# Performance work log

Hardware: AMD Instinct MI355X
Metric: run time of the kernel (lower is better)

Reference implementation:

```python
import jax, jax.numpy as jnp
from jax import lax
import numpy as np


def conv2d(x, w, b=None, stride=1, pad=0, groups=1):
    out = lax.conv_general_dilated(x, w, (stride, stride), [(pad, pad), (pad, pad)],
                                   dimension_numbers=('NCHW', 'OIHW', 'NCHW'),
                                   feature_group_count=groups)
    if b is not None:
        out = out + b[None, :, None, None]
    return out


def ln(x, g, b, eps=1e-5):
    m = x.mean(-1, keepdims=True)
    v = ((x - m) ** 2).mean(-1, keepdims=True)
    return (x - m) * lax.rsqrt(v + eps) * g + b


def grid_sample_bilinear(img, grid):
    # img [N,C,H,W]; grid [N,Hg,Wg,2] with (x,y) in [-1,1]; align_corners=True, zeros padding
    N, C, H, W = img.shape
    x = (grid[..., 0] + 1.0) * 0.5 * (W - 1)
    y = (grid[..., 1] + 1.0) * 0.5 * (H - 1)
    x0 = jnp.floor(x); y0 = jnp.floor(y)
    x1 = x0 + 1.0; y1 = y0 + 1.0
    wx1 = x - x0; wx0 = 1.0 - wx1
    wy1 = y - y0; wy0 = 1.0 - wy1
    imgh = img.transpose(0, 2, 3, 1)  # [N,H,W,C]
    bidx = jnp.arange(N)[:, None, None]
    def g(ix, iy):
        valid = (ix >= 0) & (ix <= W - 1) & (iy >= 0) & (iy <= H - 1)
        ixc = jnp.clip(ix, 0, W - 1).astype(jnp.int32)
        iyc = jnp.clip(iy, 0, H - 1).astype(jnp.int32)
        return imgh[bidx, iyc, ixc] * valid[..., None].astype(img.dtype)
    out = (g(x0, y0) * (wx0 * wy0)[..., None] + g(x1, y0) * (wx1 * wy0)[..., None]
           + g(x0, y1) * (wx0 * wy1)[..., None] + g(x1, y1) * (wx1 * wy1)[..., None])
    return out.transpose(0, 3, 1, 2)  # [N,C,Hg,Wg]


def setup_inputs() -> dict:
    key = jax.random.key(0)
    ks = iter(jax.random.split(key, 64))
    def rn(shape, s=0.02):
        return jax.random.normal(next(ks), shape, jnp.float32) * s
    B, C, H, W = 4, 512, 32, 32
    gc, hid = 256, 1024
    d = {}
    d['feat_tgt'] = jax.random.normal(next(ks), (B, C, H, W), jnp.float32)
    d['feat_ref'] = jax.random.normal(next(ks), (B, C, H, W), jnp.float32)
    d['emb_w'] = rn((C, 2 * C, 3, 3)); d['emb_b'] = jnp.zeros((C,), jnp.float32)
    d['q_w'] = rn((C, C)); d['q_b'] = jnp.zeros((C,), jnp.float32)
    d['k_w'] = rn((C, C)); d['k_b'] = jnp.zeros((C,), jnp.float32)
    d['v_w'] = rn((C, C)); d['v_b'] = jnp.zeros((C,), jnp.float32)
    d['out_w'] = rn((C, C)); d['out_b'] = jnp.zeros((C,), jnp.float32)
    d['ln1_w'] = jnp.ones((gc,), jnp.float32); d['ln1_b'] = jnp.zeros((gc,), jnp.float32)
    d['mb_n1_w'] = jnp.ones((gc,), jnp.float32); d['mb_n1_b'] = jnp.zeros((gc,), jnp.float32)
    d['mb_q_w'] = rn((gc, gc)); d['mb_q_b'] = jnp.zeros((gc,), jnp.float32)
    d['mb_kv_w'] = rn((2 * gc, gc)); d['mb_kv_b'] = jnp.zeros((2 * gc,), jnp.float32)
    d['mb_proj_w'] = rn((gc, gc)); d['mb_proj_b'] = jnp.zeros((gc,), jnp.float32)
    d['mb_n2_w'] = jnp.ones((gc,), jnp.float32); d['mb_n2_b'] = jnp.zeros((gc,), jnp.float32)
    d['mb_fc1_w'] = rn((hid, gc)); d['mb_fc1_b'] = jnp.zeros((hid,), jnp.float32)
    d['mb_dw_w'] = rn((hid, 1, 3, 3)); d['mb_dw_b'] = jnp.zeros((hid,), jnp.float32)
    d['mb_fc2_w'] = rn((gc, hid)); d['mb_fc2_b'] = jnp.zeros((gc,), jnp.float32)
    d['co_dw_w'] = rn((gc, 1, 9, 9)); d['co_dw_b'] = jnp.zeros((gc,), jnp.float32)
    d['co_ln_w'] = jnp.ones((gc,), jnp.float32); d['co_ln_b'] = jnp.zeros((gc,), jnp.float32)
    d['co_out_w'] = rn((2, gc))
    return d


def reference(feat_tgt, feat_ref, emb_w, emb_b, q_w, q_b, k_w, k_b, v_w, v_b, out_w, out_b,
              ln1_w, ln1_b, mb_n1_w, mb_n1_b, mb_q_w, mb_q_b, mb_kv_w, mb_kv_b,
              mb_proj_w, mb_proj_b, mb_n2_w, mb_n2_b, mb_fc1_w, mb_fc1_b, mb_dw_w, mb_dw_b,
              mb_fc2_w, mb_fc2_b, co_dw_w, co_dw_b, co_ln_w, co_ln_b, co_out_w):
    B, C, H, W = feat_tgt.shape
    G = 2                      # n_groups
    gc = C // G                # n_group_channels
    heads, hc = 8, C // 8      # n_heads, n_head_channels
    # embedding conv over concat(target, reference)
    feat = conv2d(jnp.concatenate([feat_tgt, feat_ref], 1), emb_w, emb_b, pad=1)
    q = jnp.einsum('bchw,oc->bohw', feat_tgt, q_w) + q_b[None, :, None, None]
    # group tokens + LN
    fg = feat.reshape(B * G, gc, H * W).transpose(0, 2, 1)  # [BG, N, gc]
    x = ln(fg, ln1_w, ln1_b)
    # ---- MitBlock offset generator ----
    BG, N, D = x.shape
    mh = 8; mhd = D // mh
    h = ln(x, mb_n1_w, mb_n1_b, 1e-6)
    qq = (h @ mb_q_w.T + mb_q_b).reshape(BG, N, mh, mhd).transpose(0, 2, 1, 3)
    kv = (h @ mb_kv_w.T + mb_kv_b).reshape(BG, N, 2, mh, mhd).transpose(2, 0, 3, 1, 4)
    kk, vv = kv[0], kv[1]
    a = jax.nn.softmax(jnp.einsum('bhnd,bhmd->bhnm', qq, kk) * (mhd ** -0.5), axis=-1)
    o = jnp.einsum('bhnm,bhmd->bhnd', a, vv).transpose(0, 2, 1, 3).reshape(BG, N, D)
    x = x + (o @ mb_proj_w.T + mb_proj_b)
    h2 = ln(x, mb_n2_w, mb_n2_b, 1e-6)
    m = h2 @ mb_fc1_w.T + mb_fc1_b                         # [BG, N, hid]
    hid = m.shape[-1]
    mi = m.transpose(0, 2, 1).reshape(BG, hid, H, W)
    mi = conv2d(mi, mb_dw_w, mb_dw_b, pad=1, groups=hid)
    m = jax.nn.gelu(mi.reshape(BG, hid, N).transpose(0, 2, 1), approximate=False)
    x = x + (m @ mb_fc2_w.T + mb_fc2_b)
    # ---- conv_offset stack ----
    off = x.reshape(BG, H, W, gc).transpose(0, 3, 1, 2)
    off = conv2d(off, co_dw_w, co_dw_b, pad=4, groups=gc)
    off = ln(off.transpose(0, 2, 3, 1), co_ln_w, co_ln_b).transpose(0, 3, 1, 2)
    off = jax.nn.gelu(off, approximate=False)
    off = jnp.einsum('bchw,oc->bohw', off, co_out_w)       # [BG, 2, Hk, Wk]
    Hk, Wk = off.shape[2], off.shape[3]
    ns = Hk * Wk
    rng = jnp.array([1.0 / Hk, 1.0 / Wk], feat.dtype).reshape(1, 2, 1, 1)
    off = jnp.tanh(off) * rng * 2.0                        # offset_range_factor = 2
    off = off.transpose(0, 2, 3, 1)                        # [BG, Hk, Wk, 2] (y,x)
    ry = (jnp.linspace(0.5, Hk - 0.5, Hk, dtype=feat.dtype) / Hk) * 2 - 1
    rx = (jnp.linspace(0.5, Wk - 0.5, Wk, dtype=feat.dtype) / Wk) * 2 - 1
    ref = jnp.stack(jnp.meshgrid(ry, rx, indexing='ij'), -1)  # [Hk, Wk, 2] (y,x)
    pos = off + ref[None]
    sampled = grid_sample_bilinear(feat.reshape(BG, gc, H, W), pos[..., ::-1])
    sampled = sampled.reshape(B, C, ns)
    k = jnp.einsum('bcn,oc->bon', sampled, k_w) + k_b[None, :, None]
    v = jnp.einsum('bcn,oc->bon', sampled, v_w) + v_b[None, :, None]
    qh = q.reshape(B * heads, hc, H * W)
    kh = k.reshape(B * heads, hc, ns)
    vh = v.reshape(B * heads, hc, ns)
    attn = jax.nn.softmax(jnp.einsum('bcm,bcn->bmn', qh, kh) * (hc ** -0.5), axis=-1)
    out = jnp.einsum('bmn,bcn->bcm', attn, vh).reshape(B, C, H, W)
    y = jnp.einsum('bchw,oc->bohw', out, out_w) + out_b[None, :, None, None]
    return y
```

## Files before the change

### kernel.cpp

```cpp
#include <hip/hip_runtime.h>
#include <math.h>


static constexpr int HW = 1024;

typedef __attribute__((ext_vector_type(8))) short bf16x8;
typedef __attribute__((ext_vector_type(4))) float f32x4;

union V16u { int4 i4; ushort u[8]; };

__device__ __forceinline__ float gelu_exact(float v) {
  return 0.5f * v * (1.0f + erff(v * 0.7071067811865475f));
}

__device__ __forceinline__ ushort bf16_rne(float v) {
  unsigned int b = __float_as_uint(v);
  return (ushort)((b + 0x7fffu + ((b >> 16) & 1u)) >> 16);
}

__device__ __forceinline__ void split2(float v, ushort& h, ushort& l) {
  h = bf16_rne(v);
  l = bf16_rne(v - __uint_as_float(((unsigned int)h) << 16));
}

__device__ __forceinline__ void wfrag_body(const float* __restrict__ W, int K, int KC,
                                           ushort* __restrict__ dh, ushort* __restrict__ dl,
                                           int gtid, float scale) {
  int l = gtid & 63; int fr = gtid >> 6;
  int kc = fr % KC; int ot = fr / KC;
  int lr = l & 15, lu = l >> 4;
  const float* sp = W + (size_t)(ot * 16 + lr) * K + kc * 32 + lu * 8;
  V16u hi, lo;
#pragma unroll
  for (int j = 0; j < 8; ++j) split2(sp[j] * scale, hi.u[j], lo.u[j]);
  *(int4*)(dh + (size_t)gtid * 8) = hi.i4;
  *(int4*)(dl + (size_t)gtid * 8) = lo.i4;
}

__global__ void k_prep_all(
    const float* __restrict__ emb_w, const float* __restrict__ tgt,
    const float* __restrict__ refp,
    const float* q_w, const float* k_w, const float* v_w, const float* o_w,
    const float* mq_w, const float* mkv_w, const float* mp_w,
    const float* f1_w, const float* f2_w, const float* dw9_w,
    const float* q_b, const float* mq_b, const float* mkv_b,
    const float* k_b, const float* v_b,
    ushort* __restrict__ WtEH, ushort* __restrict__ WtEL,
    ushort* __restrict__ XtH, ushort* __restrict__ XtL,
    ushort* qh, ushort* ql, ushort* kvh, ushort* kvl,
    ushort* oh, ushort* ol, ushort* mqkvh, ushort* mqkvl,
    ushort* mph, ushort* mpl, ushort* f1h, ushort* f1l, ushort* f2h, ushort* f2l,
    float* wt9, float* biasmb, float* biaskv, float* biasq,
    ushort* tgtfh, ushort* tgtfl) {
  int bid = blockIdx.x, tid = threadIdx.x;
  if (bid < 2048) {
    int idx = bid * 256 + tid;
    int o = idx >> 10, ci = idx & 1023;
    const float* src = emb_w + (size_t)idx * 9;
#pragma unroll
    for (int t = 0; t < 9; ++t) {
      ushort h, l; split2(src[t], h, l);
      size_t oo = ((size_t)(t * 512 + o)) * 1024 + ci;
      WtEH[oo] = h; WtEL[oo] = l;
    }
  } else if (bid < 4360) {
    int idx = (bid - 2048) * 256 + tid;
    int xp = idx % 34; int r = idx / 34;
    int g8 = r & 127; r >>= 7;
    int yp = r % 34; int b = r / 34;
    int y = yp - 1, x = xp - 1;
    bool valid = (unsigned)y < 32u && (unsigned)x < 32u;
    V16u hi, lo;
    const float* in = (g8 < 64) ? (tgt + ((size_t)(b * 512 + g8 * 8)) * HW)
                                : (refp + ((size_t)(b * 512 + (g8 - 64) * 8)) * HW);
#pragma unroll
    for (int j = 0; j < 8; ++j) {
      float v = valid ? in[(size_t)j * HW + y * 32 + x] : 0.f;
      split2(v, hi.u[j], lo.u[j]);
    }
    size_t oo = (((size_t)(b * 34 + yp)) * 34 + xp) * 1024 + g8 * 8;
    *(int4*)(XtH + oo) = hi.i4;
    *(int4*)(XtL + oo) = lo.i4;
  }
  else if (bid < 4488) wfrag_body(q_w, 512, 16, qh, ql, (bid - 4360) * 256 + tid, 0.125f);
  else if (bid < 4616) wfrag_body(k_w, 512, 16, kvh, kvl, (bid - 4488) * 256 + tid, 1.f);
  else if (bid < 4744) wfrag_body(v_w, 512, 16, kvh + 262144, kvl + 262144,
                                  (bid - 4616) * 256 + tid, 1.f);
  else if (bid < 4872) wfrag_body(o_w, 512, 16, oh, ol, (bid - 4744) * 256 + tid, 1.f);
  else if (bid < 4904) wfrag_body(mq_w, 256, 8, mqkvh, mqkvl, (bid - 4872) * 256 + tid,
                                  0.17677669529663689f);
  else if (bid < 4968) wfrag_body(mkv_w, 256, 8, mqkvh + 65536, mqkvl + 65536,
                                  (bid - 4904) * 256 + tid, 1.f);
  else if (bid < 5000) wfrag_body(mp_w, 256, 8, mph, mpl, (bid - 4968) * 256 + tid, 1.f);
  else if (bid < 5128) wfrag_body(f1_w, 256, 8, f1h, f1l, (bid - 5000) * 256 + tid, 1.f);
  else if (bid < 5256) wfrag_body(f2_w, 1024, 32, f2h, f2l, (bid - 5128) * 256 + tid, 1.f);
  else if (bid < 5337) {
    int idx = (bid - 5256) * 256 + tid;
    int t = idx >> 8, c = idx & 255;
    wt9[idx] = dw9_w[c * 81 + t];
  } else if (bid < 5346) {
    int idx = (bid - 5337) * 256 + tid;
    if (idx < 768)
      biasmb[idx] = idx < 256 ? mq_b[idx] * 0.17677669529663689f : mkv_b[idx - 256];
    else if (idx < 1792) {
      int j = idx - 768;
      biaskv[j] = j < 512 ? k_b[j] : v_b[j - 512];
    } else if (idx < 2304) {
      biasq[idx - 1792] = q_b[idx - 1792] * 0.125f;
    }
  } else {
    int gtid = (bid - 5346) * 256 + tid;
    int l = gtid & 63; int fr = gtid >> 6;
    int kc = fr % 16; int r2 = fr / 16; int nt = r2 & 63; int b = r2 >> 6;
    int lr = l & 15, lu = l >> 4;
    const float* sp = tgt + ((size_t)(b * 512) + kc * 32 + lu * 8) * 1024 + nt * 16 + lr;
    V16u hi, lo;
#pragma unroll
    for (int j = 0; j < 8; ++j) split2(sp[(size_t)j * 1024], hi.u[j], lo.u[j]);
    *(int4*)(tgtfh + (size_t)gtid * 8) = hi.i4;
    *(int4*)(tgtfl + (size_t)gtid * 8) = lo.i4;
  }
}

__global__ __launch_bounds__(256, 2)
void k_emb_mfma(const ushort* __restrict__ Xt_hi, const ushort* __restrict__ Xt_lo,
                const ushort* __restrict__ Wt_hi, const ushort* __restrict__ Wt_lo,
                float* __restrict__ part) {
  int wgid = (blockIdx.x & 7) * 64 + (blockIdx.x >> 3);
  int yt = wgid & 7;  wgid >>= 3;
  int b  = wgid & 3;  wgid >>= 2;
  int mt = wgid & 3;  wgid >>= 2;
  int ks = wgid;
  int tid = threadIdx.x;
  int w = tid >> 6, l = tid & 63;
  int lr = l & 15, lu = l >> 4;
  int y0 = yt * 4;
  int obase = mt * 128 + w * 32;

  __shared__ int4 LsH[2][816];
  __shared__ int4 LsL[2][816];

  int4 gh[4], gl[4];
  int kc0 = ks * 8;

  auto loadstage = [&](int kcg) {
#pragma unroll
    for (int i = 0; i < 4; ++i) {
      int s = tid + 256 * i;
      if (s < 816) {
        int px = s >> 2;
        int u = (s & 3) ^ ((px >> 1) & 3);
        size_t off = ((size_t)(b * 34 + y0) * 34 + px) * 1024 + kcg * 32 + u * 8;
        gh[i] = *(const int4*)(Xt_hi + off);
        gl[i] = *(const int4*)(Xt_lo + off);
      }
    }
  };
  auto writestage = [&](int buf) {
#pragma unroll
    for (int i = 0; i < 4; ++i) {
      int s = tid + 256 * i;
      if (s < 816) { LsH[buf][s] = gh[i]; LsL[buf][s] = gl[i]; }
    }
  };

  f32x4 zero = {0.f, 0.f, 0.f, 0.f};
  f32x4 acc[2][8];
#pragma unroll
  for (int a = 0; a < 2; ++a)
#pragma unroll
    for (int n = 0; n < 8; ++n) acc[a][n] = zero;

  loadstage(kc0);
  writestage(0);

  for (int kc = 0; kc < 8; ++kc) {
    int buf = kc & 1;
    __syncthreads();
    if (kc < 7) loadstage(kc0 + kc + 1);
    int kcg = kc0 + kc;
    const bf16x8* BH = (const bf16x8*)&LsH[buf][0];
    const bf16x8* BL = (const bf16x8*)&LsL[buf][0];
#pragma unroll
    for (int kx = 0; kx < 3; ++kx) {
      bf16x8 bh[12], bl[12];
#pragma unroll
      for (int f = 0; f < 12; ++f) {
        int px = (f >> 1) * 34 + (f & 1) * 16 + kx + lr;
        int idx = px * 4 + (lu ^ ((px >> 1) & 3));
        bh[f] = BH[idx]; bl[f] = BL[idx];
      }
#pragma unroll
      for (int ky = 0; ky < 3; ++ky) {
        int tap = ky * 3 + kx;
        size_t wo = (((size_t)(tap * 512 + obase + lr)) * 1024) + kcg * 32 + lu * 8;
        bf16x8 ah0 = *(const bf16x8*)(Wt_hi + wo);
        bf16x8 al0 = *(const bf16x8*)(Wt_lo + wo);
        bf16x8 ah1 = *(const bf16x8*)(Wt_hi + wo + 16 * 1024);
        bf16x8 al1 = *(const bf16x8*)(Wt_lo + wo + 16 * 1024);
#pragma unroll
        for (int yr = 0; yr < 4; ++yr)
#pragma unroll
          for (int h = 0; h < 2; ++h) {
            int f = (yr + ky) * 2 + h;
            int nf = yr * 2 + h;
            acc[0][nf] = __builtin_amdgcn_mfma_f32_16x16x32_bf16(ah0, bh[f], acc[0][nf], 0, 0, 0);
            acc[0][nf] = __builtin_amdgcn_mfma_f32_16x16x32_bf16(ah0, bl[f], acc[0][nf], 0, 0, 0);
            acc[0][nf] = __builtin_amdgcn_mfma_f32_16x16x32_bf16(al0, bh[f], acc[0][nf], 0, 0, 0);
            acc[1][nf] = __builtin_amdgcn_mfma_f32_16x16x32_bf16(ah1, bh[f], acc[1][nf], 0, 0, 0);
            acc[1][nf] = __builtin_amdgcn_mfma_f32_16x16x32_bf16(ah1, bl[f], acc[1][nf], 0, 0, 0);
            acc[1][nf] = __builtin_amdgcn_mfma_f32_16x16x32_bf16(al1, bh[f], acc[1][nf], 0, 0, 0);
          }
      }
    }
    if (kc < 7) writestage(buf ^ 1);
  }

  float* pb = part + (size_t)ks * 2097152;
#pragma unroll
  for (int a = 0; a < 2; ++a)
#pragma unroll
    for (int yr = 0; yr < 4; ++yr)
#pragma unroll
      for (int h = 0; h < 2; ++h) {
        f32x4 c = acc[a][yr * 2 + h];
        size_t base = ((size_t)(b * 512 + obase + a * 16 + lu * 4)) * 1024
                      + (y0 + yr) * 32 + h * 16 + lr;
#pragma unroll
        for (int r = 0; r < 4; ++r) pb[base + (size_t)r * 1024] = c[r];
      }
}

__global__ void k_embmerge_nc(const float* __restrict__ part, const float* __restrict__ bias,
                              float* __restrict__ featnc) {
  __shared__ float T[64][65];
  int bid = blockIdx.x;
  int n0 = (bid & 15) << 6; bid >>= 4;
  int c0 = (bid & 3) << 6; int bg = bid >> 2;
  int cl = threadIdx.x & 63, rw = threadIdx.x >> 6;
#pragma unroll
  for (int i = 0; i < 16; ++i) {
    int crow = i * 4 + rw;
    size_t idx = ((size_t)(bg * 256 + c0 + crow)) * 1024 + n0 + cl;
    float v = part[idx] + part[2097152 + idx] + part[4194304 + idx] + part[6291456 + idx];
    T[crow][cl] = v + bias[(bg & 1) * 256 + c0 + crow];
  }
  __syncthreads();
#pragma unroll
  for (int i = 0; i < 16; ++i) {
    int nrow = i * 4 + rw;
    featnc[((size_t)(bg * 1024 + n0 + nrow)) * 256 + c0 + cl] = T[cl][nrow];
  }
}

__global__ __launch_bounds__(256)
void k_gemm_mfma(const ushort* __restrict__ Ah, const ushort* __restrict__ Al,
                 const ushort* __restrict__ Bh, const ushort* __restrict__ Bl,
                 const float* __restrict__ bias, float* __restrict__ Y,
                 int KC, int MT, int Mtot) {
  int bid = blockIdx.x;
  int ntb = bid & 15; bid >>= 4;
  int mt = bid % MT; int b = bid / MT;
  int tid = threadIdx.x, w = tid >> 6, l = tid & 63, lr = l & 15, lu = l >> 4;
  int wo = w >> 1, wn = w & 1;
  int ot0 = mt * 4 + wo * 2;
  int nf0 = ntb * 4 + wn * 2;
  const bf16x8* pAh = (const bf16x8*)Ah;
  const bf16x8* pAl = (const bf16x8*)Al;
  const bf16x8* pBh = (const bf16x8*)Bh;
  const bf16x8* pBl = (const bf16x8*)Bl;
  f32x4 zero = {0.f, 0.f, 0.f, 0.f};
  f32x4 acc[2][2];
#pragma unroll
  for (int a = 0; a < 2; ++a)
#pragma unroll
    for (int n = 0; n < 2; ++n) acc[a][n] = zero;
  for (int kc = 0; kc < KC; ++kc) {
    bf16x8 a_h[2], a_l[2];
#pragma unroll
    for (int a = 0; a < 2; ++a) {
      size_t idx = ((size_t)(ot0 + a) * KC + kc) * 64 + l;
      a_h[a] = pAh[idx]; a_l[a] = pAl[idx];
    }
#pragma unroll
    for (int n = 0; n < 2; ++n) {
      size_t idx = (((size_t)(b * 64 + nf0 + n)) * KC + kc) * 64 + l;
      bf16x8 b_h = pBh[idx], b_l = pBl[idx];
#pragma unroll
      for (int a = 0; a < 2; ++a) {
        acc[a][n] = __builtin_amdgcn_mfma_f32_16x16x32_bf16(a_h[a], b_h, acc[a][n], 0, 0, 0);
        acc[a][n] = __builtin_amdgcn_mfma_f32_16x16x32_bf16(a_h[a], b_l, acc[a][n], 0, 0, 0);
        acc[a][n] = __builtin_amdgcn_mfma_f32_16x16x32_bf16(a_l[a], b_h, acc[a][n], 0, 0, 0);
      }
    }
  }
#pragma unroll
  for (int a = 0; a < 2; ++a) {
    int o = (ot0 + a) * 16 + lu * 4;
#pragma unroll
    for (int n = 0; n < 2; ++n) {
      int col = (nf0 + n) * 16 + lr;
#pragma unroll
      for (int r = 0; r < 4; ++r)
        Y[((size_t)(b * Mtot + o + r)) * 1024 + col] = acc[a][n][r] + bias[o + r];
    }
  }
}

__global__ __launch_bounds__(256)
void k_gemm_resadd(const ushort* __restrict__ Ah, const ushort* __restrict__ Al,
                   const ushort* __restrict__ Bh, const ushort* __restrict__ Bl,
                   const float* __restrict__ bias, const float* __restrict__ res,
                   float* __restrict__ dst, int KC, int MT, int addmode) {
  int bid = blockIdx.x;
  int ntb = bid & 15; bid >>= 4;
  int mt = bid % MT; int b = bid / MT;
  int tid = threadIdx.x, w = tid >> 6, l = tid & 63, lr = l & 15, lu = l >> 4;
  int wo = w >> 1, wn = w & 1;
  int ot0 = mt * 4 + wo * 2;
  int nf0 = ntb * 4 + wn * 2;
  const bf16x8* pAh = (const bf16x8*)Ah;
  const bf16x8* pAl = (const bf16x8*)Al;
  const bf16x8* pBh = (const bf16x8*)Bh;
  const bf16x8* pBl = (const bf16x8*)Bl;
  f32x4 zero = {0.f, 0.f, 0.f, 0.f};
  f32x4 acc[2][2];
#pragma unroll
  for (int a = 0; a < 2; ++a)
#pragma unroll
    for (int n = 0; n < 2; ++n) acc[a][n] = zero;
  for (int kc = 0; kc < KC; ++kc) {
    bf16x8 a_h[2], a_l[2];
#pragma unroll
    for (int a = 0; a < 2; ++a) {
      size_t idx = ((size_t)(ot0 + a) * KC + kc) * 64 + l;
      a_h[a] = pAh[idx]; a_l[a] = pAl[idx];
    }
#pragma unroll
    for (int n = 0; n < 2; ++n) {
      size_t idx = (((size_t)(b * 64 + nf0 + n)) * KC + kc) * 64 + l;
      bf16x8 b_h = pBh[idx], b_l = pBl[idx];
#pragma unroll
      for (int a = 0; a < 2; ++a) {
        acc[a][n] = __builtin_amdgcn_mfma_f32_16x16x32_bf16(a_h[a], b_h, acc[a][n], 0, 0, 0);
        acc[a][n] = __builtin_amdgcn_mfma_f32_16x16x32_bf16(a_h[a], b_l, acc[a][n], 0, 0, 0);
        acc[a][n] = __builtin_amdgcn_mfma_f32_16x16x32_bf16(a_l[a], b_h, acc[a][n], 0, 0, 0);
      }
    }
  }
#pragma unroll
  for (int a = 0; a < 2; ++a) {
    int o = (ot0 + a) * 16 + lu * 4;
#pragma unroll
    for (int n = 0; n < 2; ++n) {
      int col = (nf0 + n) * 16 + lr;
      size_t addr = ((size_t)((b << 10) + col)) * 256 + o;
      float4 v;
      v.x = acc[a][n][0] + bias[o + 0];
      v.y = acc[a][n][1] + bias[o + 1];
      v.z = acc[a][n][2] + bias[o + 2];
      v.w = acc[a][n][3] + bias[o + 3];
      float4 r4 = addmode ? *(const float4*)(dst + addr) : *(const float4*)(res + addr);
      v.x += r4.x; v.y += r4.y; v.z += r4.z; v.w += r4.w;
      *(float4*)(dst + addr) = v;
    }
  }
}

__global__ __launch_bounds__(256)
void k_gemm_frag_mb(const ushort* __restrict__ Ah, const ushort* __restrict__ Al,
                    const ushort* __restrict__ Bh, const ushort* __restrict__ Bl,
                    const float* __restrict__ bias,
                    ushort* __restrict__ mQh, ushort* __restrict__ mQl,
                    ushort* __restrict__ mKh, ushort* __restrict__ mKl,
                    ushort* __restrict__ mVh, ushort* __restrict__ mVl) {
  int bid = blockIdx.x;
  int ntb = bid & 15; bid >>= 4;
  int mt = bid % 12; int b = bid / 12;
  int tid = threadIdx.x, w = tid >> 6, l = tid & 63, lr = l & 15, lu = l >> 4;
  int wo = w >> 1, wn = w & 1;
  int ot0 = mt * 4 + wo * 2;
  int nf0 = ntb * 4 + wn * 2;
  const bf16x8* pAh = (const bf16x8*)Ah;
// ... 231 lines not shown
        den += (p0 + p1) + (p2 + p3);
        ushort h0, l0, h1, l1, h2, l2, h3, l3;
        split2(p0, h0, l0); split2(p1, h1, l1); split2(p2, h2, l2); split2(p3, h3, l3);
        uh.x = (unsigned)h0 | ((unsigned)h1 << 16); uh.y = (unsigned)h2 | ((unsigned)h3 << 16);
        ul.x = (unsigned)l0 | ((unsigned)l1 << 16); ul.y = (unsigned)l2 | ((unsigned)l3 << 16);
      }
      *(uint2*)&Ph[w][lr][kt4 * 16 + lu * 4] = uh;
      *(uint2*)&Pl[w][lr][kt4 * 16 + lu * 4] = ul;
    }
#pragma unroll
    for (int kc2 = 0; kc2 < 2; ++kc2) {
      int kc = kb * 2 + kc2;
      bf16x8 bph = *(const bf16x8*)&Ph[w][lr][kc2 * 32 + lu * 8];
      bf16x8 bpl = *(const bf16x8*)&Pl[w][lr][kc2 * 32 + lu * 8];
#pragma unroll
      for (int et = 0; et < 2; ++et) {
        bf16x8 vh = ((const bf16x8*)Vh)[(size_t)((bgh * 2 + et) * 32 + kc) * 64 + l];
        bf16x8 vl = ((const bf16x8*)Vl)[(size_t)((bgh * 2 + et) * 32 + kc) * 64 + l];
        oacc[et] = __builtin_amdgcn_mfma_f32_16x16x32_bf16(vh, bph, oacc[et], 0, 0, 0);
        oacc[et] = __builtin_amdgcn_mfma_f32_16x16x32_bf16(vh, bpl, oacc[et], 0, 0, 0);
        oacc[et] = __builtin_amdgcn_mfma_f32_16x16x32_bf16(vl, bph, oacc[et], 0, 0, 0);
      }
    }
  }
  den += __shfl_xor(den, 16);
  den += __shfl_xor(den, 32);
  float inv = 1.f / den;
  int bg = bgh >> 3, hh = bgh & 7;
#pragma unroll
  for (int et = 0; et < 2; ++et) {
    ushort4 h4, l4;
    split2(oacc[et][0] * inv, h4.x, l4.x); split2(oacc[et][1] * inv, h4.y, l4.y);
    split2(oacc[et][2] * inv, h4.z, l4.z); split2(oacc[et][3] * inv, h4.w, l4.w);
    int lu_f = et * 2 + (lu >> 1), j0 = (lu & 1) * 4;
    size_t base = ((((size_t)(bg * 64 + qt)) * 8 + hh) * 64 + lu_f * 16 + lr) * 8 + j0;
    *(ushort4*)(ofh + base) = h4;
    *(ushort4*)(ofl + base) = l4;
  }
}

__global__ __launch_bounds__(256)
void k_mainattn_mfma(const ushort* __restrict__ Qh, const ushort* __restrict__ Ql,
                     const ushort* __restrict__ Kh, const ushort* __restrict__ Kl,
                     const ushort* __restrict__ Vh, const ushort* __restrict__ Vl,
                     ushort* __restrict__ anfh, ushort* __restrict__ anfl) {
  int qb = blockIdx.x & 15, bh = blockIdx.x >> 4;
  int tid = threadIdx.x, w = tid >> 6, l = tid & 63, lr = l & 15, lu = l >> 4;
  int qt = qb * 4 + w;
  bf16x8 qh[2], ql[2];
#pragma unroll
  for (int dc = 0; dc < 2; ++dc) {
    qh[dc] = ((const bf16x8*)Qh)[(size_t)((bh * 64 + qt) * 2 + dc) * 64 + l];
    ql[dc] = ((const bf16x8*)Ql)[(size_t)((bh * 64 + qt) * 2 + dc) * 64 + l];
  }
  __shared__ ushort Ph[4][16][72];
  __shared__ ushort Pl[4][16][72];
  f32x4 zero = {0.f, 0.f, 0.f, 0.f};
  f32x4 oacc[4] = {zero, zero, zero, zero};
  float den = 0.f;
  for (int kb = 0; kb < 16; ++kb) {
#pragma unroll
    for (int kt4 = 0; kt4 < 4; ++kt4) {
      int kt = kb * 4 + kt4;
      f32x4 s = zero;
#pragma unroll
      for (int dc = 0; dc < 2; ++dc) {
        bf16x8 kh = ((const bf16x8*)Kh)[(size_t)((bh * 64 + kt) * 2 + dc) * 64 + l];
        bf16x8 kl = ((const bf16x8*)Kl)[(size_t)((bh * 64 + kt) * 2 + dc) * 64 + l];
        s = __builtin_amdgcn_mfma_f32_16x16x32_bf16(kh, qh[dc], s, 0, 0, 0);
        s = __builtin_amdgcn_mfma_f32_16x16x32_bf16(kh, ql[dc], s, 0, 0, 0);
        s = __builtin_amdgcn_mfma_f32_16x16x32_bf16(kl, qh[dc], s, 0, 0, 0);
      }
      uint2 uh, ul;
      {
        float p0 = __expf(s[0]), p1 = __expf(s[1]), p2 = __expf(s[2]), p3 = __expf(s[3]);
        den += (p0 + p1) + (p2 + p3);
        ushort h0, l0, h1, l1, h2, l2, h3, l3;
        split2(p0, h0, l0); split2(p1, h1, l1); split2(p2, h2, l2); split2(p3, h3, l3);
        uh.x = (unsigned)h0 | ((unsigned)h1 << 16); uh.y = (unsigned)h2 | ((unsigned)h3 << 16);
        ul.x = (unsigned)l0 | ((unsigned)l1 << 16); ul.y = (unsigned)l2 | ((unsigned)l3 << 16);
      }
      *(uint2*)&Ph[w][lr][kt4 * 16 + lu * 4] = uh;
      *(uint2*)&Pl[w][lr][kt4 * 16 + lu * 4] = ul;
    }
#pragma unroll
    for (int kc2 = 0; kc2 < 2; ++kc2) {
      int kc = kb * 2 + kc2;
      bf16x8 bph = *(const bf16x8*)&Ph[w][lr][kc2 * 32 + lu * 8];
      bf16x8 bpl = *(const bf16x8*)&Pl[w][lr][kc2 * 32 + lu * 8];
#pragma unroll
      for (int et = 0; et < 4; ++et) {
        bf16x8 vh = ((const bf16x8*)Vh)[(size_t)((bh * 4 + et) * 32 + kc) * 64 + l];
        bf16x8 vl = ((const bf16x8*)Vl)[(size_t)((bh * 4 + et) * 32 + kc) * 64 + l];
        oacc[et] = __builtin_amdgcn_mfma_f32_16x16x32_bf16(vh, bph, oacc[et], 0, 0, 0);
        oacc[et] = __builtin_amdgcn_mfma_f32_16x16x32_bf16(vh, bpl, oacc[et], 0, 0, 0);
        oacc[et] = __builtin_amdgcn_mfma_f32_16x16x32_bf16(vl, bph, oacc[et], 0, 0, 0);
      }
    }
  }
  den += __shfl_xor(den, 16);
  den += __shfl_xor(den, 32);
  float inv = 1.f / den;
  int b = bh >> 3, h = bh & 7;
#pragma unroll
  for (int et = 0; et < 4; ++et) {
    ushort4 h4, l4;
    split2(oacc[et][0] * inv, h4.x, l4.x); split2(oacc[et][1] * inv, h4.y, l4.y);
    split2(oacc[et][2] * inv, h4.z, l4.z); split2(oacc[et][3] * inv, h4.w, l4.w);
    int kc = h * 2 + (et >> 1);
    int lu_f = (et & 1) * 2 + (lu >> 1), j0 = (lu & 1) * 4;
    size_t base = ((((size_t)(b * 64 + qt)) * 16 + kc) * 64 + lu_f * 16 + lr) * 8 + j0;
    *(ushort4*)(anfh + base) = h4;
    *(ushort4*)(anfl + base) = l4;
  }
}

__global__ void k_dw3_frag(const float* __restrict__ X, const float* __restrict__ w,
                           const float* __restrict__ bias,
                           ushort* __restrict__ dh, ushort* __restrict__ dl) {
  int bid = blockIdx.x;
  int pch = bid & 3; bid >>= 2;
  int chg = bid & 127; int bg = bid >> 7;
  int tid = threadIdx.x;
  int n = pch * 256 + tid;
  int x = n & 31, y = n >> 5;
  int ch0 = chg * 8;
  V16u hi, lo;
#pragma unroll
  for (int jj = 0; jj < 8; ++jj) {
    int ch = ch0 + jj;
    const float* src = X + ((size_t)((bg << 10) + ch)) * HW;
    const float* wr = w + ch * 9;
    float acc = bias[ch];
#pragma unroll
    for (int ky = 0; ky < 3; ++ky) {
      int yy = y + ky - 1;
      if ((unsigned)yy < 32u) {
        const float* row = src + yy * 32;
#pragma unroll
        for (int kx = 0; kx < 3; ++kx) {
          int xx = x + kx - 1;
          if ((unsigned)xx < 32u) acc += row[xx] * wr[ky * 3 + kx];
        }
      }
    }
    split2(gelu_exact(acc), hi.u[jj], lo.u[jj]);
  }
  size_t base = ((((size_t)(bg * 64 + (n >> 4)) * 32 + (ch0 >> 5)) * 64)
                 + ((ch0 >> 3) & 3) * 16 + (n & 15)) * 8;
  *(int4*)(dh + base) = hi.i4;
  *(int4*)(dl + base) = lo.i4;
}

__global__ void k_dw9_nc(const float* __restrict__ Xnc, const float* __restrict__ wt9,
                         const float* __restrict__ bias, float* __restrict__ Ync) {
  int bid = blockIdx.x;
  int pt = bid & 127; int bg = bid >> 7;
  int tid = threadIdx.x;
  int y = pt >> 2, x0 = (pt & 3) * 8;
  float acc[8];
  float bs = bias[tid];
#pragma unroll
  for (int p = 0; p < 8; ++p) acc[p] = bs;
  const float* src = Xnc + (size_t)(bg << 10) * 256;
  for (int ky = 0; ky < 9; ++ky) {
    int yy = y + ky - 4;
    if ((unsigned)yy >= 32u) continue;
#pragma unroll
    for (int kx = 0; kx < 9; ++kx) {
      float wv = wt9[(ky * 9 + kx) * 256 + tid];
#pragma unroll
      for (int p = 0; p < 8; ++p) {
        int xx = x0 + p + kx - 4;
        if ((unsigned)xx < 32u)
          acc[p] += src[(size_t)(yy * 32 + xx) * 256 + tid] * wv;
      }
    }
  }
#pragma unroll
  for (int p = 0; p < 8; ++p)
    Ync[((size_t)((bg << 10) + y * 32 + x0 + p)) * 256 + tid] = acc[p];
}

__global__ void k_cotail_nc(const float* __restrict__ Xnc, const float* __restrict__ lnw,
                            const float* __restrict__ lnb, const float* __restrict__ w2,
                            float* __restrict__ pos) {
  int token = (blockIdx.x * 256 + threadIdx.x) >> 6;
  int lane = threadIdx.x & 63;
  float4 v4 = *(const float4*)(Xnc + (size_t)token * 256 + lane * 4);
  float s = v4.x + v4.y + v4.z + v4.w;
  float s2 = v4.x * v4.x + v4.y * v4.y + v4.z * v4.z + v4.w * v4.w;
#pragma unroll
  for (int off = 32; off; off >>= 1) { s += __shfl_xor(s, off); s2 += __shfl_xor(s2, off); }
  float mean = s * (1.f / 256.f);
  float rstd = rsqrtf(s2 * (1.f / 256.f) - mean * mean + 1e-5f);
  float4 g4 = *(const float4*)(lnw + lane * 4);
  float4 b4 = *(const float4*)(lnb + lane * 4);
  float4 wa = *(const float4*)(w2 + lane * 4);
  float4 wb = *(const float4*)(w2 + 256 + lane * 4);
  float ge0 = gelu_exact((v4.x - mean) * rstd * g4.x + b4.x);
  float ge1 = gelu_exact((v4.y - mean) * rstd * g4.y + b4.y);
  float ge2 = gelu_exact((v4.z - mean) * rstd * g4.z + b4.z);
  float ge3 = gelu_exact((v4.w - mean) * rstd * g4.w + b4.w);
  float o0 = ge0 * wa.x + ge1 * wa.y + ge2 * wa.z + ge3 * wa.w;
  float o1 = ge0 * wb.x + ge1 * wb.y + ge2 * wb.z + ge3 * wb.w;
#pragma unroll
  for (int off = 32; off; off >>= 1) { o0 += __shfl_xor(o0, off); o1 += __shfl_xor(o1, off); }
  if (lane == 0) {
    float offy = tanhf(o0) * (2.f / 32.f);
    float offx = tanhf(o1) * (2.f / 32.f);
    int n = token & 1023;
    int ky = n >> 5, kx = n & 31;
    float refy = ((ky + 0.5f) * (1.f / 32.f)) * 2.f - 1.f;
    float refx = ((kx + 0.5f) * (1.f / 32.f)) * 2.f - 1.f;
    pos[token * 2] = offx + refx;
    pos[token * 2 + 1] = offy + refy;
  }
}

__global__ void k_gsample_frag(const float* __restrict__ Xnc, const float* __restrict__ pos,
                               ushort* __restrict__ dh, ushort* __restrict__ dl) {
  int bid = blockIdx.x;
  int nch = bid & 15; int bg = bid >> 4;
  int tid = threadIdx.x;
  __shared__ int sI[4][64];
  __shared__ float sW[4][64];
  if (tid < 64) {
    int j = nch * 64 + tid;
    float gx = pos[((bg << 10) + j) * 2];
    float gy = pos[((bg << 10) + j) * 2 + 1];
    float fx = (gx + 1.f) * 0.5f * 31.f;
    float fy = (gy + 1.f) * 0.5f * 31.f;
    float x0f = floorf(fx), y0f = floorf(fy);
    int x0 = (int)x0f, y0 = (int)y0f;
    float wx1 = fx - x0f, wx0 = 1.f - wx1;
    float wy1 = fy - y0f, wy0 = 1.f - wy1;
    bool vx0 = (x0 >= 0) & (x0 <= 31);
    bool vx1 = (x0 + 1 >= 0) & (x0 + 1 <= 31);
    bool vy0 = (y0 >= 0) & (y0 <= 31);
    bool vy1 = (y0 + 1 >= 0) & (y0 + 1 <= 31);
    int cx0 = min(max(x0, 0), 31), cx1 = min(max(x0 + 1, 0), 31);
    int cy0 = min(max(y0, 0), 31), cy1 = min(max(y0 + 1, 0), 31);
    sW[0][tid] = wx0 * wy0 * ((vx0 && vy0) ? 1.f : 0.f);
    sW[1][tid] = wx1 * wy0 * ((vx1 && vy0) ? 1.f : 0.f);
    sW[2][tid] = wx0 * wy1 * ((vx0 && vy1) ? 1.f : 0.f);
    sW[3][tid] = wx1 * wy1 * ((vx1 && vy1) ? 1.f : 0.f);
    sI[0][tid] = cy0 * 32 + cx0; sI[1][tid] = cy0 * 32 + cx1;
    sI[2][tid] = cy1 * 32 + cx0; sI[3][tid] = cy1 * 32 + cx1;
  }
  __syncthreads();
  int b = bg >> 1, g = bg & 1;
  const float* src = Xnc + (size_t)(bg << 10) * 256;
  for (int nn = 0; nn < 64; ++nn) {
    float acc = src[(size_t)sI[0][nn] * 256 + tid] * sW[0][nn]
              + src[(size_t)sI[1][nn] * 256 + tid] * sW[1][nn]
              + src[(size_t)sI[2][nn] * 256 + tid] * sW[2][nn]
              + src[(size_t)sI[3][nn] * 256 + tid] * sW[3][nn];
    ushort h, l; split2(acc, h, l);
    int jglob = nch * 64 + nn;
    size_t addr = ((((size_t)(b * 64 + (jglob >> 4)) * 16) + g * 8 + (tid >> 5)) * 64
                   + ((tid >> 3) & 3) * 16 + (jglob & 15)) * 8 + (tid & 7);
    dh[addr] = h; dl[addr] = l;
  }
}

extern "C" void kernel_launch(void* const* d_in, const int* in_sizes, int n_in,
                              void* d_out, int out_size, void* d_ws, size_t ws_size,
                              hipStream_t stream) {
  const float* tgt    = (const float*)d_in[0];
  const float* refp   = (const float*)d_in[1];
  const float* emb_w  = (const float*)d_in[2];
  const float* emb_b  = (const float*)d_in[3];
  const float* q_w    = (const float*)d_in[4];
  const float* q_b    = (const float*)d_in[5];
  const float* k_w    = (const float*)d_in[6];
  const float* k_b    = (const float*)d_in[7];
  const float* v_w    = (const float*)d_in[8];
  const float* v_b    = (const float*)d_in[9];
  const float* out_w  = (const float*)d_in[10];
  const float* out_b  = (const float*)d_in[11];
  const float* ln1_w  = (const float*)d_in[12];
  const float* ln1_b  = (const float*)d_in[13];
  const float* n1_w   = (const float*)d_in[14];
  const float* n1_b   = (const float*)d_in[15];
  const float* mbq_w  = (const float*)d_in[16];
  const float* mbq_b  = (const float*)d_in[17];
  const float* mbkv_w = (const float*)d_in[18];
  const float* mbkv_b = (const float*)d_in[19];
  const float* mbp_w  = (const float*)d_in[20];
  const float* mbp_b  = (const float*)d_in[21];
  const float* n2_w   = (const float*)d_in[22];
  const float* n2_b   = (const float*)d_in[23];
  const float* fc1_w  = (const float*)d_in[24];
  const float* fc1_b  = (const float*)d_in[25];
  const float* dw3_w  = (const float*)d_in[26];
  const float* dw3_b  = (const float*)d_in[27];
  const float* fc2_w  = (const float*)d_in[28];
  const float* fc2_b  = (const float*)d_in[29];
  const float* dw9_w  = (const float*)d_in[30];
  const float* dw9_b  = (const float*)d_in[31];
  const float* coln_w = (const float*)d_in[32];
  const float* coln_b = (const float*)d_in[33];
  const float* coout_w= (const float*)d_in[34];

  float* ws = (float*)d_ws;
  float* slabA = ws + 0;
  float* qfrag = ws + 2097152;
  float* xbuf  = ws + 4194304;
  float* slabD = ws + 6291456;
  float* slabE = ws + 8388608;
  float* slabF = ws + 10485760;
  float* slabG = ws + 14680064;
  float* slabH = ws + 23068672;
  float* featnc= ws + 31457280;
  float* posb  = ws + 35389440;
  float* wt9   = ws + 35405824;
  float* biasmb= ws + 35426560;
  float* biaskv= ws + 35427328;
  float* biasq = ws + 35428352;

  ushort* XtH = (ushort*)(ws + 4194304);
  ushort* XtL = XtH + 4734976;
  ushort* WtEH = (ushort*)slabG;
  ushort* WtEL = WtEH + 4718592;
  float* part = slabH;
  ushort* tgtfh = (ushort*)slabF;
  ushort* tgtfl = tgtfh + 2097152;

  ushort* J = (ushort*)(ws + 33554432);
  ushort* wfq_h   = J;                ushort* wfq_l   = J + 262144;
  ushort* wfkv_h  = J + 524288;       ushort* wfkv_l  = J + 1048576;
  ushort* wfo_h   = J + 1572864;      ushort* wfo_l   = J + 1835008;
  ushort* wfmqkv_h= J + 2097152;      ushort* wfmqkv_l= J + 2293760;
  ushort* wfmp_h  = J + 2490368;      ushort* wfmp_l  = J + 2555904;
  ushort* wff1_h  = J + 2621440;      ushort* wff1_l  = J + 2883584;
  ushort* wff2_h  = J + 3145728;      ushort* wff2_l  = J + 3407872;

  ushort* hfh = (ushort*)slabH;     ushort* hfl = hfh + 2097152;
  ushort* mQh = (ushort*)slabG;     ushort* mQl = mQh + 2097152;
  ushort* mKh = mQh + 4194304;      ushort* mKl = mQh + 6291456;
  ushort* mVh = mQh + 8388608;      ushort* mVl = mQh + 10485760;
  ushort* ofh = (ushort*)slabF;     ushort* ofl = ofh + 2097152;
  ushort* h2fh = (ushort*)slabF;    ushort* h2fl = h2fh + 2097152;
  float* m_cm = slabG;
  ushort* mifh = (ushort*)slabH;    ushort* mifl = mifh + 8388608;
  float* offin = slabA;
  float* offdwnc = slabE;
  ushort* sfh = (ushort*)slabF;     ushort* sfl = sfh + 2097152;
  ushort* aQh = (ushort*)qfrag;     ushort* aQl = aQh + 2097152;
  ushort* aKh = (ushort*)slabG;     ushort* aKl = aKh + 2097152;
  ushort* aVh = aKh + 4194304;      ushort* aVl = aKh + 6291456;
  ushort* anfh = (ushort*)slabH;    ushort* anfl = anfh + 2097152;

  k_prep_all<<<6370, 256, 0, stream>>>(
      emb_w, tgt, refp, q_w, k_w, v_w, out_w, mbq_w, mbkv_w, mbp_w, fc1_w, fc2_w,
      dw9_w, q_b, mbq_b, mbkv_b, k_b, v_b,
      WtEH, WtEL, XtH, XtL,
      wfq_h, wfq_l, wfkv_h, wfkv_l, wfo_h, wfo_l, wfmqkv_h, wfmqkv_l,
      wfmp_h, wfmp_l, wff1_h, wff1_l, wff2_h, wff2_l,
      wt9, biasmb, biaskv, biasq, tgtfh, tgtfl);
  k_emb_mfma<<<512, 256, 0, stream>>>(XtH, XtL, WtEH, WtEL, part);
  k_embmerge_nc<<<512, 256, 0, stream>>>(part, emb_b, featnc);
  k_gemm_frag_main<<<512, 256, 0, stream>>>(wfq_h, wfq_l, tgtfh, tgtfl, biasq,
                                            aQh, aQl, aVh, aVl, 512, 16, 8);
  k_ln1n1<<<2048, 256, 0, stream>>>(featnc, ln1_w, ln1_b, n1_w, n1_b, xbuf, hfh, hfl);
  k_gemm_frag_mb<<<1536, 256, 0, stream>>>(wfmqkv_h, wfmqkv_l, hfh, hfl, biasmb,
                                           mQh, mQl, mKh, mKl, mVh, mVl);
  k_mbattn_mfma<<<1024, 256, 0, stream>>>(mQh, mQl, mKh, mKl, mVh, mVl, ofh, ofl);
  k_gemm_resadd<<<512, 256, 0, stream>>>(wfmp_h, wfmp_l, ofh, ofl, mbp_b,
                                         xbuf, xbuf, 8, 4, 1);
  k_ln_frag<<<2048, 256, 0, stream>>>(xbuf, n2_w, n2_b, h2fh, h2fl, 1e-6f);
  k_gemm_mfma<<<2048, 256, 0, stream>>>(wff1_h, wff1_l, h2fh, h2fl, fc1_b, m_cm, 8, 16, 1024);
  k_dw3_frag<<<4096, 256, 0, stream>>>(m_cm, dw3_w, dw3_b, mifh, mifl);
  k_gemm_resadd<<<512, 256, 0, stream>>>(wff2_h, wff2_l, mifh, mifl, fc2_b,
                                         xbuf, offin, 32, 4, 0);
  k_dw9_nc<<<1024, 256, 0, stream>>>(offin, wt9, dw9_b, offdwnc);
  k_cotail_nc<<<2048, 256, 0, stream>>>(offdwnc, coln_w, coln_b, coout_w, posb);
  k_gsample_frag<<<128, 256, 0, stream>>>(featnc, posb, sfh, sfl);
  k_gemm_frag_main<<<1024, 256, 0, stream>>>(wfkv_h, wfkv_l, sfh, sfl, biaskv,
                                             aKh, aKl, aVh, aVl, 512, 16, 16);
  k_mainattn_mfma<<<512, 256, 0, stream>>>(aQh, aQl, aKh, aKl, aVh, aVl, anfh, anfl);
  k_gemm_mfma<<<512, 256, 0, stream>>>(wfo_h, wfo_l, anfh, anfl, out_b, (float*)d_out, 16, 8, 512);
}
```

Baseline: 554.0 us.

## Shrink emb conv tiles for higher occupancy and fuse dw9 with offset tail

The embedding conv MFMA kernel now has each wave compute 16 output channels instead of 32. It drops LDS double buffering, doubles the grid to 1024 blocks and raises launch bounds to 4 waves per SIMD, trading per-block data reuse and load/compute overlap for occupancy. Separately, the 9x9 depthwise conv is fused with the LayerNorm/GELU/projection/tanh offset tail. This removes an intermediate buffer round trip and one kernel launch, at the cost of block-level shared-memory reductions and extra syncs.

```diff
diff --git a/kernel.cpp b/kernel.cpp
--- a/kernel.cpp
+++ b/kernel.cpp
@@ -122,23 +122,23 @@
   }
 }
 
-__global__ __launch_bounds__(256, 2)
+__global__ __launch_bounds__(256, 4)
 void k_emb_mfma(const ushort* __restrict__ Xt_hi, const ushort* __restrict__ Xt_lo,
                 const ushort* __restrict__ Wt_hi, const ushort* __restrict__ Wt_lo,
                 float* __restrict__ part) {
-  int wgid = (blockIdx.x & 7) * 64 + (blockIdx.x >> 3);
+  int wgid = (blockIdx.x & 7) * 128 + (blockIdx.x >> 3);
   int yt = wgid & 7;  wgid >>= 3;
   int b  = wgid & 3;  wgid >>= 2;
-  int mt = wgid & 3;  wgid >>= 2;
-  int ks = wgid;
+  int ks = wgid & 3;  wgid >>= 2;
+  int mt = wgid;
   int tid = threadIdx.x;
   int w = tid >> 6, l = tid & 63;
   int lr = l & 15, lu = l >> 4;
   int y0 = yt * 4;
-  int obase = mt * 128 + w * 32;
-
-  __shared__ int4 LsH[2][816];
-  __shared__ int4 LsL[2][816];
+  int obase = mt * 64 + w * 16;
+
+  __shared__ int4 LsH[816];
+  __shared__ int4 LsL[816];
 
   int4 gh[4], gl[4];
   int kc0 = ks * 8;
@@ -156,31 +156,28 @@
       }
     }
   };
-  auto writestage = [&](int buf) {
+  auto writestage = [&]() {
 #pragma unroll
     for (int i = 0; i < 4; ++i) {
       int s = tid + 256 * i;
-      if (s < 816) { LsH[buf][s] = gh[i]; LsL[buf][s] = gl[i]; }
+      if (s < 816) { LsH[s] = gh[i]; LsL[s] = gl[i]; }
     }
   };
 
   f32x4 zero = {0.f, 0.f, 0.f, 0.f};
-  f32x4 acc[2][8];
-#pragma unroll
-  for (int a = 0; a < 2; ++a)
-#pragma unroll
-    for (int n = 0; n < 8; ++n) acc[a][n] = zero;
+  f32x4 acc[8];
+#pragma unroll
+  for (int n = 0; n < 8; ++n) acc[n] = zero;
 
   loadstage(kc0);
-  writestage(0);
+  writestage();
 
   for (int kc = 0; kc < 8; ++kc) {
-    int buf = kc & 1;
     __syncthreads();
     if (kc < 7) loadstage(kc0 + kc + 1);
     int kcg = kc0 + kc;
-    const bf16x8* BH = (const bf16x8*)&LsH[buf][0];
-    const bf16x8* BL = (const bf16x8*)&LsL[buf][0];
+    const bf16x8* BH = (const bf16x8*)&LsH[0];
+    const bf16x8* BL = (const bf16x8*)&LsL[0];
 #pragma unroll
     for (int kx = 0; kx < 3; ++kx) {
       bf16x8 bh[12], bl[12];
@@ -194,41 +191,37 @@
       for (int ky = 0; ky < 3; ++ky) {
         int tap = ky * 3 + kx;
         size_t wo = (((size_t)(tap * 512 + obase + lr)) * 1024) + kcg * 32 + lu * 8;
-        bf16x8 ah0 = *(const bf16x8*)(Wt_hi + wo);
-        bf16x8 al0 = *(const bf16x8*)(Wt_lo + wo);
-        bf16x8 ah1 = *(const bf16x8*)(Wt_hi + wo + 16 * 1024);
-        bf16x8 al1 = *(const bf16x8*)(Wt_lo + wo + 16 * 1024);
+        bf16x8 ah = *(const bf16x8*)(Wt_hi + wo);
+        bf16x8 al = *(const bf16x8*)(Wt_lo + wo);
 #pragma unroll
         for (int yr = 0; yr < 4; ++yr)
 #pragma unroll
           for (int h = 0; h < 2; ++h) {
             int f = (yr + ky) * 2 + h;
             int nf = yr * 2 + h;
-            acc[0][nf] = __builtin_amdgcn_mfma_f32_16x16x32_bf16(ah0, bh[f], acc[0][nf], 0, 0, 0);
-            acc[0][nf] = __builtin_amdgcn_mfma_f32_16x16x32_bf16(ah0, bl[f], acc[0][nf], 0, 0, 0);
-            acc[0][nf] = __builtin_amdgcn_mfma_f32_16x16x32_bf16(al0, bh[f], acc[0][nf], 0, 0, 0);
-            acc[1][nf] = __builtin_amdgcn_mfma_f32_16x16x32_bf16(ah1, bh[f], acc[1][nf], 0, 0, 0);
-            acc[1][nf] = __builtin_amdgcn_mfma_f32_16x16x32_bf16(ah1, bl[f], acc[1][nf], 0, 0, 0);
-            acc[1][nf] = __builtin_amdgcn_mfma_f32_16x16x32_bf16(al1, bh[f], acc[1][nf], 0, 0, 0);
+            acc[nf] = __builtin_amdgcn_mfma_f32_16x16x32_bf16(ah, bh[f], acc[nf], 0, 0, 0);
+            acc[nf] = __builtin_amdgcn_mfma_f32_16x16x32_bf16(ah, bl[f], acc[nf], 0, 0, 0);
+            acc[nf] = __builtin_amdgcn_mfma_f32_16x16x32_bf16(al, bh[f], acc[nf], 0, 0, 0);
           }
       }
     }
-    if (kc < 7) writestage(buf ^ 1);
+    if (kc < 7) {
+      __syncthreads();
+      writestage();
+    }
   }
 
   float* pb = part + (size_t)ks * 2097152;
 #pragma unroll
-  for (int a = 0; a < 2; ++a)
-#pragma unroll
-    for (int yr = 0; yr < 4; ++yr)
-#pragma unroll
-      for (int h = 0; h < 2; ++h) {
-        f32x4 c = acc[a][yr * 2 + h];
-        size_t base = ((size_t)(b * 512 + obase + a * 16 + lu * 4)) * 1024
-                      + (y0 + yr) * 32 + h * 16 + lr;
-#pragma unroll
-        for (int r = 0; r < 4; ++r) pb[base + (size_t)r * 1024] = c[r];
-      }
+  for (int yr = 0; yr < 4; ++yr)
+#pragma unroll
+    for (int h = 0; h < 2; ++h) {
+      f32x4 c = acc[yr * 2 + h];
+      size_t base = ((size_t)(b * 512 + obase + lu * 4)) * 1024
+                    + (y0 + yr) * 32 + h * 16 + lr;
+#pragma unroll
+      for (int r = 0; r < 4; ++r) pb[base + (size_t)r * 1024] = c[r];
+    }
 }
 
 __global__ void k_embmerge_nc(const float* __restrict__ part, const float* __restrict__ bias,
@@ -766,8 +759,10 @@
   *(int4*)(dl + base) = lo.i4;
 }
 
-__global__ void k_dw9_nc(const float* __restrict__ Xnc, const float* __restrict__ wt9,
-                         const float* __restrict__ bias, float* __restrict__ Ync) {
+__global__ void k_dw9cotail(const float* __restrict__ Xnc, const float* __restrict__ wt9,
+                            const float* __restrict__ bias,
+                            const float* __restrict__ lnw, const float* __restrict__ lnb,
+                            const float* __restrict__ w2, float* __restrict__ pos) {
   int bid = blockIdx.x;
   int pt = bid & 127; int bg = bid >> 7;
   int tid = threadIdx.x;
@@ -791,44 +786,42 @@
       }
     }
   }
-#pragma unroll
-  for (int p = 0; p < 8; ++p)
-    Ync[((size_t)((bg << 10) + y * 32 + x0 + p)) * 256 + tid] = acc[p];
-}
-
-__global__ void k_cotail_nc(const float* __restrict__ Xnc, const float* __restrict__ lnw,
-                            const float* __restrict__ lnb, const float* __restrict__ w2,
-                            float* __restrict__ pos) {
-  int token = (blockIdx.x * 256 + threadIdx.x) >> 6;
-  int lane = threadIdx.x & 63;
-  float4 v4 = *(const float4*)(Xnc + (size_t)token * 256 + lane * 4);
-  float s = v4.x + v4.y + v4.z + v4.w;
-  float s2 = v4.x * v4.x + v4.y * v4.y + v4.z * v4.z + v4.w * v4.w;
-#pragma unroll
-  for (int off = 32; off; off >>= 1) { s += __shfl_xor(s, off); s2 += __shfl_xor(s2, off); }
-  float mean = s * (1.f / 256.f);
-  float rstd = rsqrtf(s2 * (1.f / 256.f) - mean * mean + 1e-5f);
-  float4 g4 = *(const float4*)(lnw + lane * 4);
-  float4 b4 = *(const float4*)(lnb + lane * 4);
-  float4 wa = *(const float4*)(w2 + lane * 4);
-  float4 wb = *(const float4*)(w2 + 256 + lane * 4);
-  float ge0 = gelu_exact((v4.x - mean) * rstd * g4.x + b4.x);
-  float ge1 = gelu_exact((v4.y - mean) * rstd * g4.y + b4.y);
-  float ge2 = gelu_exact((v4.z - mean) * rstd * g4.z + b4.z);
-  float ge3 = gelu_exact((v4.w - mean) * rstd * g4.w + b4.w);
-  float o0 = ge0 * wa.x + ge1 * wa.y + ge2 * wa.z + ge3 * wa.w;
-  float o1 = ge0 * wb.x + ge1 * wb.y + ge2 * wb.z + ge3 * wb.w;
-#pragma unroll
-  for (int off = 32; off; off >>= 1) { o0 += __shfl_xor(o0, off); o1 += __shfl_xor(o1, off); }
-  if (lane == 0) {
+  __shared__ float rs[8][4], rs2[8][4], ro0[8][4], ro1[8][4];
+  int wv = tid >> 6, ln = tid & 63;
+  float lw = lnw[tid], lb = lnb[tid];
+  float wa = w2[tid], wb = w2[256 + tid];
+#pragma unroll
+  for (int p = 0; p < 8; ++p) {
+    float a = acc[p], b2 = acc[p] * acc[p];
+#pragma unroll
+    for (int off = 32; off; off >>= 1) { a += __shfl_xor(a, off); b2 += __shfl_xor(b2, off); }
+    if (ln == 0) { rs[p][wv] = a; rs2[p][wv] = b2; }
+  }
+  __syncthreads();
+#pragma unroll
+  for (int p = 0; p < 8; ++p) {
+    float tot  = rs[p][0] + rs[p][1] + rs[p][2] + rs[p][3];
+    float tot2 = rs2[p][0] + rs2[p][1] + rs2[p][2] + rs2[p][3];
+    float mean = tot * (1.f / 256.f);
+    float rstd = rsqrtf(tot2 * (1.f / 256.f) - mean * mean + 1e-5f);
+    float ge = gelu_exact((acc[p] - mean) * rstd * lw + lb);
+    float o0 = ge * wa, o1 = ge * wb;
+#pragma unroll
+    for (int off = 32; off; off >>= 1) { o0 += __shfl_xor(o0, off); o1 += __shfl_xor(o1, off); }
+    if (ln == 0) { ro0[p][wv] = o0; ro1[p][wv] = o1; }
+  }
+  __syncthreads();
+  if (tid < 8) {
+    int p = tid;
+    float o0 = ro0[p][0] + ro0[p][1] + ro0[p][2] + ro0[p][3];
+    float o1 = ro1[p][0] + ro1[p][1] + ro1[p][2] + ro1[p][3];
     float offy = tanhf(o0) * (2.f / 32.f);
     float offx = tanhf(o1) * (2.f / 32.f);
-    int n = token & 1023;
-    int ky = n >> 5, kx = n & 31;
-    float refy = ((ky + 0.5f) * (1.f / 32.f)) * 2.f - 1.f;
-    float refx = ((kx + 0.5f) * (1.f / 32.f)) * 2.f - 1.f;
-    pos[token * 2] = offx + refx;
-    pos[token * 2 + 1] = offy + refy;
+    int n = y * 32 + x0 + p;
+    float refy = ((y + 0.5f) * (1.f / 32.f)) * 2.f - 1.f;
+    float refx = ((x0 + p + 0.5f) * (1.f / 32.f)) * 2.f - 1.f;
+    pos[((bg << 10) + n) * 2]     = offx + refx;
+    pos[((bg << 10) + n) * 2 + 1] = offy + refy;
   }
 }
 
@@ -921,8 +914,6 @@
   float* slabA = ws + 0;
   float* qfrag = ws + 2097152;
   float* xbuf  = ws + 4194304;
-  float* slabD = ws + 6291456;
-  float* slabE = ws + 8388608;
   float* slabF = ws + 10485760;
   float* slabG = ws + 14680064;
   float* slabH = ws + 23068672;
@@ -959,7 +950,6 @@
   float* m_cm = slabG;
   ushort* mifh = (ushort*)slabH;    ushort* mifl = mifh + 8388608;
   float* offin = slabA;
-  float* offdwnc = slabE;
   ushort* sfh = (ushort*)slabF;     ushort* sfl = sfh + 2097152;
   ushort* aQh = (ushort*)qfrag;     ushort* aQl = aQh + 2097152;
   ushort* aKh = (ushort*)slabG;     ushort* aKl = aKh + 2097152;
@@ -973,7 +963,7 @@
       wfq_h, wfq_l, wfkv_h, wfkv_l, wfo_h, wfo_l, wfmqkv_h, wfmqkv_l,
       wfmp_h, wfmp_l, wff1_h, wff1_l, wff2_h, wff2_l,
       wt9, biasmb, biaskv, biasq, tgtfh, tgtfl);
-  k_emb_mfma<<<512, 256, 0, stream>>>(XtH, XtL, WtEH, WtEL, part);
+  k_emb_mfma<<<1024, 256, 0, stream>>>(XtH, XtL, WtEH, WtEL, part);
   k_embmerge_nc<<<512, 256, 0, stream>>>(part, emb_b, featnc);
   k_gemm_frag_main<<<512, 256, 0, stream>>>(wfq_h, wfq_l, tgtfh, tgtfl, biasq,
                                             aQh, aQl, aVh, aVl, 512, 16, 8);
@@ -988,8 +978,7 @@
   k_dw3_frag<<<4096, 256, 0, stream>>>(m_cm, dw3_w, dw3_b, mifh, mifl);
   k_gemm_resadd<<<512, 256, 0, stream>>>(wff2_h, wff2_l, mifh, mifl, fc2_b,
                                          xbuf, offin, 32, 4, 0);
-  k_dw9_nc<<<1024, 256, 0, stream>>>(offin, wt9, dw9_b, offdwnc);
-  k_cotail_nc<<<2048, 256, 0, stream>>>(offdwnc, coln_w, coln_b, coout_w, posb);
+  k_dw9cotail<<<1024, 256, 0, stream>>>(offin, wt9, dw9_b, coln_w, coln_b, coout_w, posb);
   k_gsample_frag<<<128, 256, 0, stream>>>(featnc, posb, sfh, sfl);
   k_gemm_frag_main<<<1024, 256, 0, stream>>>(wfkv_h, wfkv_l, sfh, sfl, biaskv,
                                              aKh, aKl, aVh, aVl, 512, 16, 16);
```

Result: slower. 630.2 us (+13.8%).
